# Optimization experiments

Hardware: AMD Instinct MI355X
Metric: run time of the kernel (lower is better)

## Reference

```python
import jax, jax.numpy as jnp
import numpy as np

H = 128      # hidden_size
L = 2        # num_layers
IN0 = 96     # seq_feature_size + context_feature_size
OUT = 1

def _xavier(k, shape):
    fan_out, fan_in = shape
    lim = (6.0 / (fan_in + fan_out)) ** 0.5
    return jax.random.uniform(k, shape, jnp.float32, -lim, lim)

def _orth(k, n):
    q, _ = jnp.linalg.qr(jax.random.normal(k, (n, n)))
    return q.astype(jnp.float32)

def setup_inputs() -> dict:
    key = jax.random.key(0)
    ks = jax.random.split(key, 16)
    B, S, F_seq, F_ctx = 512, 512, 64, 32
    inp = {
        "seq_features": jax.random.normal(ks[0], (B, S, F_seq), jnp.float32),
        "context_features": jax.random.normal(ks[1], (B, F_ctx), jnp.float32),
    }
    for i in range(L):
        in_size = IN0 if i == 0 else H
        inp[f"tau{i}"] = jax.random.normal(ks[2 + 5 * i], (H,), jnp.float32) * 0.1
        inp[f"Win{i}"] = _xavier(ks[3 + 5 * i], (H, in_size))
        inp[f"Wrec{i}"] = _orth(ks[4 + 5 * i], H)
        inp[f"Wg{i}"] = _xavier(ks[5 + 5 * i], (H, in_size + H))
        inp[f"bg{i}"] = jnp.zeros((H,), jnp.float32)
    inp["W1"] = _xavier(ks[12], (H // 2, H))
    inp["b1"] = jnp.zeros((H // 2,), jnp.float32)
    inp["W2"] = _xavier(ks[13], (OUT, H // 2))
    inp["b2"] = jnp.zeros((OUT,), jnp.float32)
    return inp

def _cell_step(x, h, tau_p, Win, Wrec, Wg, bg):
    # LTC cell: RK4 integration of dh/dt = -h/tau + W_in x + gate * W_rec h
    tau = jax.nn.softplus(tau_p) + 1.0
    def rhs(hh):
        gate = jax.nn.sigmoid(jnp.tanh(jnp.concatenate([x, hh], axis=-1) @ Wg.T + bg))
        return -hh / tau + x @ Win.T + gate * (hh @ Wrec.T)
    k1 = rhs(h)
    k2 = rhs(h + 0.5 * k1)
    k3 = rhs(h + 0.5 * k2)
    k4 = rhs(h + k3)
    return jnp.tanh(h + (k1 + 2.0 * k2 + 2.0 * k3 + k4) / 6.0)

def reference(seq_features, context_features, tau0, Win0, Wrec0, Wg0, bg0,
              tau1, Win1, Wrec1, Wg1, bg1, W1, b1, W2, b2):
    B, S, _ = seq_features.shape
    ctx = jnp.broadcast_to(context_features[:, None, :], (B, S, context_features.shape[-1]))
    x = jnp.concatenate([seq_features, ctx], axis=-1)     # [B,S,IN0]
    xs = jnp.swapaxes(x, 0, 1)                            # [S,B,IN0] time-major
    cells = [(tau0, Win0, Wrec0, Wg0, bg0), (tau1, Win1, Wrec1, Wg1, bg1)]
    h_init = tuple(jnp.zeros((B, H), x.dtype) for _ in range(L))

    def step(hs, xt):
        new = []
        inp = xt
        for hi, p in zip(hs, cells):
            hn = _cell_step(inp, hi, *p)
            new.append(hn)
            inp = hn
        return tuple(new), None

    hs, _ = jax.lax.scan(step, h_init, xs)
    h_last = hs[-1]                                       # [B,H]
    # classifier (dropout is identity in eval mode)
    out = jax.nn.sigmoid(jax.nn.relu(h_last @ W1.T + b1) @ W2.T + b2)
    return out.reshape(B, -1)
```

## Files before the change

### kernel.cpp

```cpp
#include <hip/hip_runtime.h>


typedef _Float16 f16;
typedef _Float16 f16x4 __attribute__((ext_vector_type(4)));
typedef _Float16 f16x8 __attribute__((ext_vector_type(8)));
typedef float f32x4 __attribute__((ext_vector_type(4)));

#define NSTEP 512
#define OFF_A0 0
#define OFF_A1 32768
#define OFF_AIO 65536
#define OFF_AX 98304
#define W_TOTAL 122880

#define HQ0 0
#define HQ1 4352
#define L0A 8704
#define L0B 13056
#define L1A 17408
#define L1B 21760
#define L1H 26112
#define XT 30464

__device__ __forceinline__ float rcp_f(float x) { return __builtin_amdgcn_rcpf(x); }
__device__ __forceinline__ float tanh_f(float x) {
  float e = __expf(2.f * x);
  return 1.f - 2.f * rcp_f(e + 1.f);
}
__device__ __forceinline__ float sig_poly(float t) {
  float s = t * t;
  float p = fmaf(s, 2.1356861e-5f, -2.1081349e-4f);
  p = fmaf(s, p, 2.0833333e-3f);
  p = fmaf(s, p, -2.0833333e-2f);
  p = fmaf(s, p, 0.25f);
  return fmaf(t, p, 0.5f);
}

__global__ __launch_bounds__(256) void prep_kernel(
    const float* __restrict__ Win0, const float* __restrict__ Wrec0,
    const float* __restrict__ Wg0, const float* __restrict__ Win1,
    const float* __restrict__ Wrec1, const float* __restrict__ Wg1,
    f16* __restrict__ W) {
  int i = blockIdx.x * 256 + threadIdx.x;
  if (i >= W_TOTAL) return;
  if (i < OFF_AX) {
    int sec = i >> 15;
    int r = i & 32767;
    int j = r & 7, lane = (r >> 3) & 63, kc = (r >> 9) & 3, sel = (r >> 11) & 1,
        w = (r >> 12) & 7;
    int row = w * 16 + (lane & 15);
    int k = kc * 32 + ((lane >> 4) << 3) + j;
    float v;
    if (sec == 0)
      v = sel ? Wrec0[row * 128 + k] : Wg0[row * 224 + 96 + k];
    else if (sec == 1)
      v = sel ? Wrec1[row * 128 + k] : Wg1[row * 256 + 128 + k];
    else
      v = sel ? Wg1[row * 256 + k] : Win1[row * 128 + k];
    W[i] = (f16)v;
  } else {
    int r = i - OFF_AX;
    int j = r & 7, lane = (r >> 3) & 63, g = r >> 9;
    int kc = g % 3, sg = g / 3;
    int sel = sg & 1, w = sg >> 1;
    int row = w * 16 + (lane & 15);
    int k = kc * 32 + ((lane >> 4) << 3) + j;
    W[i] = (f16)(sel ? Wg0[row * 224 + k] : Win0[row * 96 + k]);
  }
}

#define MFMA16(A, B, C) __builtin_amdgcn_mfma_f32_16x16x32_f16((A), (B), (C), 0, 0, 0)
#define ZERO4 ((f32x4){0.f, 0.f, 0.f, 0.f})

#define MM2(SRC)                                                    \
  {                                                                 \
    const f16* bp_ = (SRC) + c * 136 + 8 * q;                       \
    _Pragma("unroll") for (int kc_ = 0; kc_ < 4; ++kc_) {           \
      f16x8 bf_ = *(const f16x8*)(bp_ + kc_ * 32);                  \
      ga[0] = MFMA16(awg[0][kc_], bf_, ga[0]);                      \
      ra[0] = MFMA16(awr[0][kc_], bf_, ra[0]);                      \
      ga[1] = MFMA16(awg[1][kc_], bf_, ga[1]);                      \
      ra[1] = MFMA16(awr[1][kc_], bf_, ra[1]);                      \
    }                                                               \
  }

#define MMIO(SRC, KCN)                                              \
  {                                                                 \
    const f16* bp_ = (SRC) + c * 136 + 8 * q;                       \
    _Pragma("unroll") for (int kc_ = 0; kc_ < (KCN); ++kc_) {       \
      f16x8 bf_ = *(const f16x8*)(bp_ + kc_ * 32);                  \
      ga[0] = MFMA16(au[0][kc_], bf_, ga[0]);                       \
      ra[0] = MFMA16(ag2[0][kc_], bf_, ra[0]);                      \
      ga[1] = MFMA16(au[1][kc_], bf_, ga[1]);                       \
      ra[1] = MFMA16(ag2[1][kc_], bf_, ra[1]);                      \
    }                                                               \
  }

#define GATEALL(WC, HC, DST)                                        \
  _Pragma("unroll") for (int i2_ = 0; i2_ < 2; ++i2_) {             \
    f16x4 hv_;                                                      \
    _Pragma("unroll") for (int r_ = 0; r_ < 4; ++r_) {              \
      float th_ = tanh_f(ga[i2_][r_] + gx[i2_][r_]);                \
      float gt_ = sig_poly(th_);                                    \
      float kk_ = fmaf(gt_, ra[i2_][r_],                            \
                       fmaf(-itv[i2_][r_], hhc[i2_][r_], u[i2_][r_])); \
      ksum[i2_][r_] = fmaf((WC), kk_, ksum[i2_][r_]);               \
      float hn_ = fmaf((HC), kk_, hst[i2_][r_]);                    \
      hhc[i2_][r_] = hn_;                                           \
      hv_[r_] = (f16)hn_;                                           \
    }                                                               \
    *(f16x4*)((DST) + c * 136 + jb[i2_]) = hv_;                     \
  }

#define GATEFIN(DST)                                                \
  _Pragma("unroll") for (int i2_ = 0; i2_ < 2; ++i2_) {             \
    f16x4 hv_;                                                      \
    _Pragma("unroll") for (int r_ = 0; r_ < 4; ++r_) {              \
      float th_ = tanh_f(ga[i2_][r_] + gx[i2_][r_]);                \
      float gt_ = sig_poly(th_);                                    \
      float kk_ = fmaf(gt_, ra[i2_][r_],                            \
                       fmaf(-itv[i2_][r_], hhc[i2_][r_], u[i2_][r_])); \
      float ks_ = ksum[i2_][r_] + kk_;                              \
      float hn_ = tanh_f(fmaf(ks_, 0.16666667f, hst[i2_][r_]));     \
      hst[i2_][r_] = hn_;                                           \
      hhc[i2_][r_] = hn_;                                           \
      hv_[r_] = (f16)hn_;                                           \
    }                                                               \
    *(f16x4*)((DST) + c * 136 + jb[i2_]) = hv_;                     \
  }

#define ZACC { ga[0] = ZERO4; ra[0] = ZERO4; ga[1] = ZERO4; ra[1] = ZERO4; }

__global__ __launch_bounds__(512, 2) void ltc_kernel(
    const float* __restrict__ seq, const float* __restrict__ ctx,
    const float* __restrict__ tau0p, const float* __restrict__ bg0p,
    const float* __restrict__ tau1p, const float* __restrict__ bg1p,
    const float* __restrict__ W1, const float* __restrict__ b1,
    const float* __restrict__ W2, const float* __restrict__ b2,
    const f16* __restrict__ W, float* __restrict__ out) {
  __shared__ __align__(16) char smem[32768];
  f16* hq0 = (f16*)(smem + HQ0);
  f16* hq1 = (f16*)(smem + HQ1);
  f16* l0a = (f16*)(smem + L0A);
  f16* l0b = (f16*)(smem + L0B);
  f16* l1a = (f16*)(smem + L1A);
  f16* l1b = (f16*)(smem + L1B);
  f16* l1h = (f16*)(smem + L1H);
  f16* xt = (f16*)(smem + XT);

  const int tid = threadIdx.x;
  const int w8 = tid >> 6, lane = tid & 63;
  const int q = lane >> 4, c = lane & 15;
  const int wl = w8 & 3;
  const bool isL0 = (w8 < 4);
  const int bg = blockIdx.x;
  int jb[2];
  jb[0] = 32 * wl + 4 * q;
  jb[1] = jb[0] + 16;

  f16* bufA = isL0 ? l0a : l1a;
  f16* bufB = isL0 ? l0b : l1b;

  f16x8 awg[2][4], awr[2][4], au[2][4], ag2[2][4];
  f16x8 bctx;
  if (isL0) {
#pragma unroll
    for (int i2 = 0; i2 < 2; ++i2) {
      int T = 2 * wl + i2;
#pragma unroll
      for (int kc = 0; kc < 4; ++kc) {
        awg[i2][kc] = *(const f16x8*)(W + OFF_A0 + (((T * 2 + 0) * 4 + kc) * 64 + lane) * 8);
        awr[i2][kc] = *(const f16x8*)(W + OFF_A0 + (((T * 2 + 1) * 4 + kc) * 64 + lane) * 8);
      }
#pragma unroll
      for (int kc = 0; kc < 3; ++kc) {
        au[i2][kc] = *(const f16x8*)(W + OFF_AX + (((T * 2 + 0) * 3 + kc) * 64 + lane) * 8);
        ag2[i2][kc] = *(const f16x8*)(W + OFF_AX + (((T * 2 + 1) * 3 + kc) * 64 + lane) * 8);
      }
      au[i2][3] = (f16x8)(f16)0.f;
      ag2[i2][3] = (f16x8)(f16)0.f;
    }
    const float* cp = ctx + (bg * 16 + c) * 32 + 8 * q;
#pragma unroll
    for (int j = 0; j < 8; ++j) bctx[j] = (f16)cp[j];
  } else {
#pragma unroll
    for (int i2 = 0; i2 < 2; ++i2) {
      int T = 2 * wl + i2;
#pragma unroll
      for (int kc = 0; kc < 4; ++kc) {
        awg[i2][kc] = *(const f16x8*)(W + OFF_A1 + (((T * 2 + 0) * 4 + kc) * 64 + lane) * 8);
        awr[i2][kc] = *(const f16x8*)(W + OFF_A1 + (((T * 2 + 1) * 4 + kc) * 64 + lane) * 8);
        au[i2][kc] = *(const f16x8*)(W + OFF_AIO + (((T * 2 + 0) * 4 + kc) * 64 + lane) * 8);
        ag2[i2][kc] = *(const f16x8*)(W + OFF_AIO + (((T * 2 + 1) * 4 + kc) * 64 + lane) * 8);
      }
    }
  }

  const float* taup = isL0 ? tau0p : tau1p;
  const float* bgp = isL0 ? bg0p : bg1p;
  f32x4 itv[2], bgv[2];
#pragma unroll
  for (int i2 = 0; i2 < 2; ++i2)
#pragma unroll
    for (int r = 0; r < 4; ++r) {
      float t = taup[jb[i2] + r];
      itv[i2][r] = 1.f / (logf(1.f + __expf(t)) + 1.f);
      bgv[i2][r] = bgp[jb[i2] + r];
    }

  f32x4 hst[2], hhc[2], u[2], gx[2], ksum[2], ga[2], ra[2];
  hst[0] = hst[1] = hhc[0] = hhc[1] = ZERO4;
  ksum[0] = ksum[1] = ZERO4;

  for (int j = tid; j < 2176; j += 512) {
    hq1[j] = (f16)0.f;
    l1h[j] = (f16)0.f;
  }
  const int bs = tid >> 4, fp = tid & 15;
  const size_t seqrow = ((size_t)(bg * 16 + bs)) * NSTEP * 64 + 4 * fp;
  if (tid < 256) {
    float4 sv = *(const float4*)(seq + seqrow);
    *(f16x4*)(xt + bs * 72 + 4 * fp) =
        (f16x4){(f16)sv.x, (f16)sv.y, (f16)sv.z, (f16)sv.w};
  }
  __syncthreads();

  float4 sqv = {0.f, 0.f, 0.f, 0.f};

#pragma unroll 1
  for (int i = 0; i <= NSTEP; ++i) {
    const f16* hprev = ((i + 1) & 1) ? hq1 : hq0;

    if (isL0) {
      if (i < NSTEP) {
        if (i + 1 < NSTEP) sqv = *(const float4*)(seq + seqrow + (size_t)(i + 1) * 64);
        ZACC;
        {
          f16x8 bx0 = *(const f16x8*)(xt + c * 72 + 8 * q);
          f16x8 bx1 = *(const f16x8*)(xt + c * 72 + 32 + 8 * q);
#pragma unroll
          for (int i2 = 0; i2 < 2; ++i2) {
            ga[i2] = MFMA16(au[i2][0], bx0, ga[i2]);
            ra[i2] = MFMA16(ag2[i2][0], bx0, ra[i2]);
            ga[i2] = MFMA16(au[i2][1], bx1, ga[i2]);
            ra[i2] = MFMA16(ag2[i2][1], bx1, ra[i2]);
            ga[i2] = MFMA16(au[i2][2], bctx, ga[i2]);
            ra[i2] = MFMA16(ag2[i2][2], bctx, ra[i2]);
          }
        }
#pragma unroll
        for (int i2 = 0; i2 < 2; ++i2) {
          u[i2] = ga[i2];
#pragma unroll
          for (int r = 0; r < 4; ++r) gx[i2][r] = ra[i2][r] + bgv[i2][r];
        }
        ZACC;
        MM2(hprev);
        ksum[0] = ZERO4; ksum[1] = ZERO4;
        GATEALL(1.0f, 0.5f, bufA);
      }
    } else {
      if (i >= 1) {
        ZACC;
        MMIO(hprev, 4);
#pragma unroll
        for (int i2 = 0; i2 < 2; ++i2) {
          u[i2] = ga[i2];
#pragma unroll
          for (int r = 0; r < 4; ++r) gx[i2][r] = ra[i2][r] + bgv[i2][r];
        }
        ZACC;
        MM2(l1h);
        ksum[0] = ZERO4; ksum[1] = ZERO4;
        GATEALL(1.0f, 0.5f, bufA);
      }
    }
    __syncthreads();

    if ((isL0 && i < NSTEP) || (!isL0 && i >= 1)) {
      ZACC;
      MM2(bufA);
      GATEALL(2.0f, 0.5f, bufB);
    }
    __syncthreads();

    if ((isL0 && i < NSTEP) || (!isL0 && i >= 1)) {
      ZACC;
      MM2(bufB);
      GATEALL(2.0f, 1.0f, bufA);
    }
    __syncthreads();

    if (isL0) {
      if (i < NSTEP) {
        ZACC;
        MM2(bufA);
        GATEFIN((i & 1) ? hq1 : hq0);
        if (tid < 256 && i + 1 < NSTEP)
          *(f16x4*)(xt + bs * 72 + 4 * fp) =
              (f16x4){(f16)sqv.x, (f16)sqv.y, (f16)sqv.z, (f16)sqv.w};
      }
    } else {
      if (i >= 1) {
        ZACC;
        MM2(bufA);
        GATEFIN(l1h);
      }
    }
    __syncthreads();
  }

  float* h1f = (float*)smem;
  if (!isL0) {
#pragma unroll
    for (int i2 = 0; i2 < 2; ++i2)
      *(f32x4*)(h1f + c * 132 + jb[i2]) = hst[i2];
  }
  __syncthreads();
  float* z1 = (float*)(smem + 16 * 132 * 4);
  {
    int b = tid >> 5, o = tid & 31;
#pragma unroll
    for (int hlf = 0; hlf < 2; ++hlf) {
      int oo = o + 32 * hlf;
      const float* wr = W1 + oo * 128;
      const float* hr = h1f + b * 132;
      float s = 0.f;
#pragma unroll
      for (int j = 0; j < 128; j += 4) {
        f32x4 wv = *(const f32x4*)(wr + j);
        f32x4 hv = *(const f32x4*)(hr + j);
        s += wv[0] * hv[0] + wv[1] * hv[1] + wv[2] * hv[2] + wv[3] * hv[3];
      }
      s += b1[oo];
      z1[b * 64 + oo] = fmaxf(s, 0.f);
    }
  }
  __syncthreads();
  if (tid < 16) {
    float s = b2[0];
#pragma unroll
    for (int o = 0; o < 64; ++o) s += z1[tid * 64 + o] * W2[o];
    out[bg * 16 + tid] = rcp_f(1.f + __expf(-s));
  }
}

extern "C" void kernel_launch(void* const* d_in, const int* in_sizes, int n_in,
                              void* d_out, int out_size, void* d_ws, size_t ws_size,
                              hipStream_t stream) {
  (void)in_sizes; (void)n_in; (void)out_size; (void)ws_size;
  const float* seq = (const float*)d_in[0];
  const float* ctx = (const float*)d_in[1];
  const float* tau0 = (const float*)d_in[2];
  const float* Win0 = (const float*)d_in[3];
  const float* Wrec0 = (const float*)d_in[4];
  const float* Wg0 = (const float*)d_in[5];
  const float* bg0 = (const float*)d_in[6];
  const float* tau1 = (const float*)d_in[7];
  const float* Win1 = (const float*)d_in[8];
  const float* Wrec1 = (const float*)d_in[9];
  const float* Wg1 = (const float*)d_in[10];
  const float* bg1 = (const float*)d_in[11];
  const float* W1 = (const float*)d_in[12];
  const float* b1 = (const float*)d_in[13];
  const float* W2 = (const float*)d_in[14];
  const float* b2 = (const float*)d_in[15];
  f16* W = (f16*)d_ws;

  prep_kernel<<<480, 256, 0, stream>>>(Win0, Wrec0, Wg0, Win1, Wrec1, Wg1, W);
  ltc_kernel<<<32, 512, 0, stream>>>(seq, ctx, tau0, bg0, tau1, bg1, W1, b1, W2,
                                     b2, W, (float*)d_out);
}
```

Baseline: 1.963 ms.

## Split each block's work across 16 waves, one output tile per wave

Doubles the block size from 512 to 1024 threads so each wave handles a single 16-column hidden tile instead of two. This halves the serial MFMA chain and gate math per wave on each latency-bound recurrent step, spreading it across more SIMDs. In exchange, barriers now span 16 waves, and launch bounds drop the 2-blocks-per-CU hint, which may change register allocation. The classifier head is remapped so each thread computes one output.

```diff
diff --git a/kernel.cpp b/kernel.cpp
--- a/kernel.cpp
+++ b/kernel.cpp
@@ -77,10 +77,8 @@
     const f16* bp_ = (SRC) + c * 136 + 8 * q;                       \
     _Pragma("unroll") for (int kc_ = 0; kc_ < 4; ++kc_) {           \
       f16x8 bf_ = *(const f16x8*)(bp_ + kc_ * 32);                  \
-      ga[0] = MFMA16(awg[0][kc_], bf_, ga[0]);                      \
-      ra[0] = MFMA16(awr[0][kc_], bf_, ra[0]);                      \
-      ga[1] = MFMA16(awg[1][kc_], bf_, ga[1]);                      \
-      ra[1] = MFMA16(awr[1][kc_], bf_, ra[1]);                      \
+      ga = MFMA16(awg[kc_], bf_, ga);                               \
+      ra = MFMA16(awr[kc_], bf_, ra);                               \
     }                                                               \
   }
 
@@ -89,49 +87,45 @@
     const f16* bp_ = (SRC) + c * 136 + 8 * q;                       \
     _Pragma("unroll") for (int kc_ = 0; kc_ < (KCN); ++kc_) {       \
       f16x8 bf_ = *(const f16x8*)(bp_ + kc_ * 32);                  \
-      ga[0] = MFMA16(au[0][kc_], bf_, ga[0]);                       \
-      ra[0] = MFMA16(ag2[0][kc_], bf_, ra[0]);                      \
-      ga[1] = MFMA16(au[1][kc_], bf_, ga[1]);                       \
-      ra[1] = MFMA16(ag2[1][kc_], bf_, ra[1]);                      \
+      ga = MFMA16(au[kc_], bf_, ga);                                \
+      ra = MFMA16(ag2[kc_], bf_, ra);                               \
     }                                                               \
   }
 
 #define GATEALL(WC, HC, DST)                                        \
-  _Pragma("unroll") for (int i2_ = 0; i2_ < 2; ++i2_) {             \
+  {                                                                 \
     f16x4 hv_;                                                      \
     _Pragma("unroll") for (int r_ = 0; r_ < 4; ++r_) {              \
-      float th_ = tanh_f(ga[i2_][r_] + gx[i2_][r_]);                \
+      float th_ = tanh_f(ga[r_] + gx[r_]);                          \
       float gt_ = sig_poly(th_);                                    \
-      float kk_ = fmaf(gt_, ra[i2_][r_],                            \
-                       fmaf(-itv[i2_][r_], hhc[i2_][r_], u[i2_][r_])); \
-      ksum[i2_][r_] = fmaf((WC), kk_, ksum[i2_][r_]);               \
-      float hn_ = fmaf((HC), kk_, hst[i2_][r_]);                    \
-      hhc[i2_][r_] = hn_;                                           \
+      float kk_ = fmaf(gt_, ra[r_], fmaf(-itv[r_], hhc[r_], u[r_]));\
+      ksum[r_] = fmaf((WC), kk_, ksum[r_]);                         \
+      float hn_ = fmaf((HC), kk_, hst[r_]);                         \
+      hhc[r_] = hn_;                                                \
       hv_[r_] = (f16)hn_;                                           \
     }                                                               \
-    *(f16x4*)((DST) + c * 136 + jb[i2_]) = hv_;                     \
+    *(f16x4*)((DST) + c * 136 + jb) = hv_;                          \
   }
 
 #define GATEFIN(DST)                                                \
-  _Pragma("unroll") for (int i2_ = 0; i2_ < 2; ++i2_) {             \
+  {                                                                 \
     f16x4 hv_;                                                      \
     _Pragma("unroll") for (int r_ = 0; r_ < 4; ++r_) {              \
-      float th_ = tanh_f(ga[i2_][r_] + gx[i2_][r_]);                \
+      float th_ = tanh_f(ga[r_] + gx[r_]);                          \
       float gt_ = sig_poly(th_);                                    \
-      float kk_ = fmaf(gt_, ra[i2_][r_],                            \
-                       fmaf(-itv[i2_][r_], hhc[i2_][r_], u[i2_][r_])); \
-      float ks_ = ksum[i2_][r_] + kk_;                              \
-      float hn_ = tanh_f(fmaf(ks_, 0.16666667f, hst[i2_][r_]));     \
-      hst[i2_][r_] = hn_;                                           \
-      hhc[i2_][r_] = hn_;                                           \
+      float kk_ = fmaf(gt_, ra[r_], fmaf(-itv[r_], hhc[r_], u[r_]));\
+      float ks_ = ksum[r_] + kk_;                                   \
+      float hn_ = tanh_f(fmaf(ks_, 0.16666667f, hst[r_]));          \
+      hst[r_] = hn_;                                                \
+      hhc[r_] = hn_;                                                \
       hv_[r_] = (f16)hn_;                                           \
     }                                                               \
-    *(f16x4*)((DST) + c * 136 + jb[i2_]) = hv_;                     \
-  }
-
-#define ZACC { ga[0] = ZERO4; ra[0] = ZERO4; ga[1] = ZERO4; ra[1] = ZERO4; }
-
-__global__ __launch_bounds__(512, 2) void ltc_kernel(
+    *(f16x4*)((DST) + c * 136 + jb) = hv_;                          \
+  }
+
+#define ZACC { ga = ZERO4; ra = ZERO4; }
+
+__global__ __launch_bounds__(1024) void ltc_kernel(
     const float* __restrict__ seq, const float* __restrict__ ctx,
     const float* __restrict__ tau0p, const float* __restrict__ bg0p,
     const float* __restrict__ tau1p, const float* __restrict__ bg1p,
@@ -149,76 +143,62 @@
   f16* xt = (f16*)(smem + XT);
 
   const int tid = threadIdx.x;
-  const int w8 = tid >> 6, lane = tid & 63;
+  const int w16 = tid >> 6, lane = tid & 63;
   const int q = lane >> 4, c = lane & 15;
-  const int wl = w8 & 3;
-  const bool isL0 = (w8 < 4);
+  const int wl = w16 & 7;
+  const bool isL0 = (w16 < 8);
   const int bg = blockIdx.x;
-  int jb[2];
-  jb[0] = 32 * wl + 4 * q;
-  jb[1] = jb[0] + 16;
+  const int jb = 16 * wl + 4 * q;
 
   f16* bufA = isL0 ? l0a : l1a;
   f16* bufB = isL0 ? l0b : l1b;
 
-  f16x8 awg[2][4], awr[2][4], au[2][4], ag2[2][4];
+  f16x8 awg[4], awr[4], au[4], ag2[4];
   f16x8 bctx;
   if (isL0) {
 #pragma unroll
-    for (int i2 = 0; i2 < 2; ++i2) {
-      int T = 2 * wl + i2;
-#pragma unroll
-      for (int kc = 0; kc < 4; ++kc) {
-        awg[i2][kc] = *(const f16x8*)(W + OFF_A0 + (((T * 2 + 0) * 4 + kc) * 64 + lane) * 8);
-        awr[i2][kc] = *(const f16x8*)(W + OFF_A0 + (((T * 2 + 1) * 4 + kc) * 64 + lane) * 8);
-      }
-#pragma unroll
-      for (int kc = 0; kc < 3; ++kc) {
-        au[i2][kc] = *(const f16x8*)(W + OFF_AX + (((T * 2 + 0) * 3 + kc) * 64 + lane) * 8);
-        ag2[i2][kc] = *(const f16x8*)(W + OFF_AX + (((T * 2 + 1) * 3 + kc) * 64 + lane) * 8);
-      }
-      au[i2][3] = (f16x8)(f16)0.f;
-      ag2[i2][3] = (f16x8)(f16)0.f;
-    }
+    for (int kc = 0; kc < 4; ++kc) {
+      awg[kc] = *(const f16x8*)(W + OFF_A0 + (((wl * 2 + 0) * 4 + kc) * 64 + lane) * 8);
+      awr[kc] = *(const f16x8*)(W + OFF_A0 + (((wl * 2 + 1) * 4 + kc) * 64 + lane) * 8);
+    }
+#pragma unroll
+    for (int kc = 0; kc < 3; ++kc) {
+      au[kc] = *(const f16x8*)(W + OFF_AX + (((wl * 2 + 0) * 3 + kc) * 64 + lane) * 8);
+      ag2[kc] = *(const f16x8*)(W + OFF_AX + (((wl * 2 + 1) * 3 + kc) * 64 + lane) * 8);
+    }
+    au[3] = (f16x8)(f16)0.f;
+    ag2[3] = (f16x8)(f16)0.f;
     const float* cp = ctx + (bg * 16 + c) * 32 + 8 * q;
 #pragma unroll
     for (int j = 0; j < 8; ++j) bctx[j] = (f16)cp[j];
   } else {
 #pragma unroll
-    for (int i2 = 0; i2 < 2; ++i2) {
-      int T = 2 * wl + i2;
-#pragma unroll
-      for (int kc = 0; kc < 4; ++kc) {
-        awg[i2][kc] = *(const f16x8*)(W + OFF_A1 + (((T * 2 + 0) * 4 + kc) * 64 + lane) * 8);
-        awr[i2][kc] = *(const f16x8*)(W + OFF_A1 + (((T * 2 + 1) * 4 + kc) * 64 + lane) * 8);
-        au[i2][kc] = *(const f16x8*)(W + OFF_AIO + (((T * 2 + 0) * 4 + kc) * 64 + lane) * 8);
-        ag2[i2][kc] = *(const f16x8*)(W + OFF_AIO + (((T * 2 + 1) * 4 + kc) * 64 + lane) * 8);
-      }
+    for (int kc = 0; kc < 4; ++kc) {
+      awg[kc] = *(const f16x8*)(W + OFF_A1 + (((wl * 2 + 0) * 4 + kc) * 64 + lane) * 8);
+      awr[kc] = *(const f16x8*)(W + OFF_A1 + (((wl * 2 + 1) * 4 + kc) * 64 + lane) * 8);
+      au[kc] = *(const f16x8*)(W + OFF_AIO + (((wl * 2 + 0) * 4 + kc) * 64 + lane) * 8);
+      ag2[kc] = *(const f16x8*)(W + OFF_AIO + (((wl * 2 + 1) * 4 + kc) * 64 + lane) * 8);
     }
   }
 
   const float* taup = isL0 ? tau0p : tau1p;
   const float* bgp = isL0 ? bg0p : bg1p;
-  f32x4 itv[2], bgv[2];
-#pragma unroll
-  for (int i2 = 0; i2 < 2; ++i2)
-#pragma unroll
-    for (int r = 0; r < 4; ++r) {
-      float t = taup[jb[i2] + r];
-      itv[i2][r] = 1.f / (logf(1.f + __expf(t)) + 1.f);
-      bgv[i2][r] = bgp[jb[i2] + r];
-    }
-
-  f32x4 hst[2], hhc[2], u[2], gx[2], ksum[2], ga[2], ra[2];
-  hst[0] = hst[1] = hhc[0] = hhc[1] = ZERO4;
-  ksum[0] = ksum[1] = ZERO4;
-
-  for (int j = tid; j < 2176; j += 512) {
+  f32x4 itv, bgv;
+#pragma unroll
+  for (int r = 0; r < 4; ++r) {
+    float t = taup[jb + r];
+    itv[r] = 1.f / (logf(1.f + __expf(t)) + 1.f);
+    bgv[r] = bgp[jb + r];
+  }
+
+  f32x4 hst = ZERO4, hhc = ZERO4, u = ZERO4, gx = ZERO4, ksum = ZERO4, ga, ra;
+
+  for (int j = tid; j < 2176; j += 1024) {
     hq1[j] = (f16)0.f;
     l1h[j] = (f16)0.f;
   }
   const int bs = tid >> 4, fp = tid & 15;
-  const size_t seqrow = ((size_t)(bg * 16 + bs)) * NSTEP * 64 + 4 * fp;
+  const size_t seqrow = ((size_t)(bg * 16 + (bs & 15))) * NSTEP * 64 + 4 * fp;
   if (tid < 256) {
     float4 sv = *(const float4*)(seq + seqrow);
     *(f16x4*)(xt + bs * 72 + 4 * fp) =
@@ -234,45 +214,37 @@
 
     if (isL0) {
       if (i < NSTEP) {
-        if (i + 1 < NSTEP) sqv = *(const float4*)(seq + seqrow + (size_t)(i + 1) * 64);
+        if (tid < 256 && i + 1 < NSTEP)
+          sqv = *(const float4*)(seq + seqrow + (size_t)(i + 1) * 64);
         ZACC;
         {
           f16x8 bx0 = *(const f16x8*)(xt + c * 72 + 8 * q);
           f16x8 bx1 = *(const f16x8*)(xt + c * 72 + 32 + 8 * q);
-#pragma unroll
-          for (int i2 = 0; i2 < 2; ++i2) {
-            ga[i2] = MFMA16(au[i2][0], bx0, ga[i2]);
-            ra[i2] = MFMA16(ag2[i2][0], bx0, ra[i2]);
-            ga[i2] = MFMA16(au[i2][1], bx1, ga[i2]);
-            ra[i2] = MFMA16(ag2[i2][1], bx1, ra[i2]);
-            ga[i2] = MFMA16(au[i2][2], bctx, ga[i2]);
-            ra[i2] = MFMA16(ag2[i2][2], bctx, ra[i2]);
-          }
+          ga = MFMA16(au[0], bx0, ga);
+          ra = MFMA16(ag2[0], bx0, ra);
+          ga = MFMA16(au[1], bx1, ga);
+          ra = MFMA16(ag2[1], bx1, ra);
+          ga = MFMA16(au[2], bctx, ga);
+          ra = MFMA16(ag2[2], bctx, ra);
         }
-#pragma unroll
-        for (int i2 = 0; i2 < 2; ++i2) {
-          u[i2] = ga[i2];
-#pragma unroll
-          for (int r = 0; r < 4; ++r) gx[i2][r] = ra[i2][r] + bgv[i2][r];
-        }
+        u = ga;
+#pragma unroll
+        for (int r = 0; r < 4; ++r) gx[r] = ra[r] + bgv[r];
         ZACC;
         MM2(hprev);
-        ksum[0] = ZERO4; ksum[1] = ZERO4;
+        ksum = ZERO4;
         GATEALL(1.0f, 0.5f, bufA);
       }
     } else {
       if (i >= 1) {
         ZACC;
         MMIO(hprev, 4);
-#pragma unroll
-        for (int i2 = 0; i2 < 2; ++i2) {
-          u[i2] = ga[i2];
-#pragma unroll
-          for (int r = 0; r < 4; ++r) gx[i2][r] = ra[i2][r] + bgv[i2][r];
-        }
+        u = ga;
+#pragma unroll
+        for (int r = 0; r < 4; ++r) gx[r] = ra[r] + bgv[r];
         ZACC;
         MM2(l1h);
-        ksum[0] = ZERO4; ksum[1] = ZERO4;
+        ksum = ZERO4;
         GATEALL(1.0f, 0.5f, bufA);
       }
     }
@@ -312,30 +284,22 @@
   }
 
   float* h1f = (float*)smem;
-  if (!isL0) {
-#pragma unroll
-    for (int i2 = 0; i2 < 2; ++i2)
-      *(f32x4*)(h1f + c * 132 + jb[i2]) = hst[i2];
-  }
+  if (!isL0) *(f32x4*)(h1f + c * 132 + jb) = hst;
   __syncthreads();
   float* z1 = (float*)(smem + 16 * 132 * 4);
   {
-    int b = tid >> 5, o = tid & 31;
-#pragma unroll
-    for (int hlf = 0; hlf < 2; ++hlf) {
-      int oo = o + 32 * hlf;
-      const float* wr = W1 + oo * 128;
-      const float* hr = h1f + b * 132;
-      float s = 0.f;
-#pragma unroll
-      for (int j = 0; j < 128; j += 4) {
-        f32x4 wv = *(const f32x4*)(wr + j);
-        f32x4 hv = *(const f32x4*)(hr + j);
-        s += wv[0] * hv[0] + wv[1] * hv[1] + wv[2] * hv[2] + wv[3] * hv[3];
-      }
-      s += b1[oo];
-      z1[b * 64 + oo] = fmaxf(s, 0.f);
-    }
+    int b = tid >> 6, o = tid & 63;
+    const float* wr = W1 + o * 128;
+    const float* hr = h1f + b * 132;
+    float s = 0.f;
+#pragma unroll
+    for (int j = 0; j < 128; j += 4) {
+      f32x4 wv = *(const f32x4*)(wr + j);
+      f32x4 hv = *(const f32x4*)(hr + j);
+      s += wv[0] * hv[0] + wv[1] * hv[1] + wv[2] * hv[2] + wv[3] * hv[3];
+    }
+    s += b1[o];
+    z1[b * 64 + o] = fmaxf(s, 0.f);
   }
   __syncthreads();
   if (tid < 16) {
@@ -369,6 +333,6 @@
   f16* W = (f16*)d_ws;
 
   prep_kernel<<<480, 256, 0, stream>>>(Win0, Wrec0, Wg0, Win1, Wrec1, Wg1, W);
-  ltc_kernel<<<32, 512, 0, stream>>>(seq, ctx, tau0, bg0, tau1, bg1, W1, b1, W2,
-                                     b2, W, (float*)d_out);
-}
+  ltc_kernel<<<32, 1024, 0, stream>>>(seq, ctx, tau0, bg0, tau1, bg1, W1, b1, W2,
+                                      b2, W, (float*)d_out);
+}
```

New measurement: 2.248 ms. 14.5% more time.
